# Kernel optimization log

Measured on AMD Instinct MI355X. Metric: run time of the kernel, lower is better.

## Reference

```python
import jax, jax.numpy as jnp
import numpy as np

HIDDEN = 1024
INNER = 1024
LR = 0.01
EPS = 1e-5


def _layernorm(x, gamma, beta):
    mu = jnp.mean(x, axis=-1, keepdims=True)
    var = jnp.var(x, axis=-1, keepdims=True)
    return (x - mu) * jax.lax.rsqrt(var + EPS) * gamma + beta


def setup_inputs() -> dict:
    key = jax.random.key(0)
    ks = jax.random.split(key, 8)
    B, S, H, I = 64, 512, HIDDEN, INNER
    x = jax.random.normal(ks[0], (B, S, H), dtype=jnp.float32)
    W_init = jax.random.normal(ks[1], (H, I), dtype=jnp.float32) * 0.02
    b_init = jnp.zeros((I,), dtype=jnp.float32)
    # Linear weights stored as (in, out) so y = x @ W + b
    lim_t = 1.0 / np.sqrt(H)
    Wt = jax.random.uniform(ks[2], (H, I), jnp.float32, -lim_t, lim_t)
    bt = jnp.zeros((I,), dtype=jnp.float32)
    lim_o = 1.0 / np.sqrt(I)
    Wo = jax.random.uniform(ks[3], (I, H), jnp.float32, -lim_o, lim_o)
    bo = jnp.zeros((H,), dtype=jnp.float32)
    lim_g = 1.0 / np.sqrt(2 * H)
    Wg = jax.random.uniform(ks[4], (2 * H, H), jnp.float32, -lim_g, lim_g)
    bg = jnp.zeros((H,), dtype=jnp.float32)
    gamma = jnp.ones((H,), dtype=jnp.float32)
    beta = jnp.zeros((H,), dtype=jnp.float32)
    return {"x": x, "W_init": W_init, "b_init": b_init, "Wt": Wt, "bt": bt,
            "Wo": Wo, "bo": bo, "Wg": Wg, "bg": bg, "gamma": gamma, "beta": beta}


def reference(x, W_init, b_init, Wt, bt, Wo, bo, Wg, bg, gamma, beta):
    B, S, H = x.shape
    I = W_init.shape[1]
    W0 = jnp.broadcast_to(W_init[None], (B, H, I))  # per-batch fast weights
    b0 = jnp.broadcast_to(b_init[None], (B, I))

    def step(carry, x_t):
        W, b = carry
        inner = jnp.einsum('bh,bhi->bi', x_t, W) + b          # [B, I]
        ttt = jax.nn.silu(inner) @ Wo + bo                    # [B, H]
        g = jax.nn.sigmoid(jnp.concatenate([x_t, ttt], axis=-1) @ Wg + bg)
        out = _layernorm(g * ttt + (1.0 - g) * x_t, gamma, beta)
        # test-time training update (target detached)
        target = jax.lax.stop_gradient(x_t @ Wt + bt)
        err = inner - target                                   # [B, I]
        W = W - (LR / I) * x_t[:, :, None] * err[:, None, :]
        b = b - (LR / I) * err
        return (W, b), out

    xs = jnp.swapaxes(x, 0, 1)  # [S, B, H]
    (_, _), ys = jax.lax.scan(step, (W0, b0), xs)
    return jnp.swapaxes(ys, 0, 1)  # [B, S, H]
```

## Files before the change

kernel.cpp:

```cpp
#include <hip/hip_runtime.h>

#define HD 1024
#define ID 1024
#define BATCH 64
#define SEQ 512
#define BS (BATCH*SEQ)
#define CHUNK 64
#define NCHUNK (SEQ/CHUNK)
#define LR_OVER_I (0.01f/1024.0f)

typedef unsigned int u32;
typedef unsigned short ushort_t;
typedef __attribute__((ext_vector_type(8))) short short8;
typedef __attribute__((ext_vector_type(8))) unsigned short ushort8;
typedef __attribute__((ext_vector_type(4))) unsigned short ushort4v;
typedef __attribute__((ext_vector_type(4))) float floatx4;

__device__ inline ushort_t f2bf(float f) {
    union { float f; u32 u; } v; v.f = f;
    return (ushort_t)((v.u + 0x7FFFu + ((v.u >> 16) & 1u)) >> 16);
}
__device__ inline float bf2f(ushort_t h) {
    union { u32 u; float f; } v; v.u = ((u32)h) << 16; return v.f;
}

__device__ inline void load_lds16(const void* g, void* l) {
    __builtin_amdgcn_global_load_lds(
        (const __attribute__((address_space(1))) u32*)g,
        (__attribute__((address_space(3))) u32*)l, 16, 0, 0);
}

__global__ void prep_all(const float* __restrict__ x, ushort_t* __restrict__ xb,
                         const float* __restrict__ Wi, const float* __restrict__ Wt,
                         ushort_t* __restrict__ WdT, ushort_t* __restrict__ WtT,
                         const float* __restrict__ bi, const float* __restrict__ bt,
                         float* __restrict__ bd,
                         const float* __restrict__ Wo, const float* __restrict__ Wg,
                         ushort_t* __restrict__ WoT, ushort_t* __restrict__ WgT)
{
    __shared__ float t1[32][33], t2[32][33];
    int bid = blockIdx.x;
    const int tid = threadIdx.x;
    if (bid < 16384) {
        long i = ((long)bid * 256 + tid) * 8;
        float4 a = *(const float4*)(x + i);
        float4 b = *(const float4*)(x + i + 4);
        ushort8 o;
        o[0] = f2bf(a.x); o[1] = f2bf(a.y); o[2] = f2bf(a.z); o[3] = f2bf(a.w);
        o[4] = f2bf(b.x); o[5] = f2bf(b.y); o[6] = f2bf(b.z); o[7] = f2bf(b.w);
        *(ushort8*)(xb + i) = o;
        return;
    }
    bid -= 16384;
    const int tx = tid & 31, ty = tid >> 5;
    if (bid < 1024) {
        if (bid == 0)
            for (int i = tid; i < ID; i += 256) bd[i] = bi[i] - bt[i];
        int r0 = (bid >> 5) * 32, c0 = (bid & 31) * 32;
        for (int i = ty; i < 32; i += 8) {
            t1[i][tx] = Wi[(long)(r0 + i) * ID + c0 + tx];
            t2[i][tx] = Wt[(long)(r0 + i) * ID + c0 + tx];
        }
        __syncthreads();
        for (int i = ty; i < 32; i += 8) {
            float wi = t1[tx][i], wt = t2[tx][i];
            WdT[(long)(c0 + i) * HD + r0 + tx] = f2bf(wi - wt);
            WtT[(long)(c0 + i) * HD + r0 + tx] = f2bf(wt);
        }
        return;
    }
    bid -= 1024;
    int z = bid >> 10, tile = bid & 1023;
    const float* in; ushort_t* outp; int ldo;
    if (z == 0)      { in = Wo;                 outp = WoT;      ldo = ID; }
    else if (z == 1) { in = Wg;                 outp = WgT;      ldo = 2 * HD; }
    else             { in = Wg + (long)HD * HD; outp = WgT + HD; ldo = 2 * HD; }
    int r0 = (tile >> 5) * 32, c0 = (tile & 31) * 32;
    for (int i = ty; i < 32; i += 8)
        t1[i][tx] = in[(long)(r0 + i) * HD + c0 + tx];
    __syncthreads();
    for (int i = ty; i < 32; i += 8)
        outp[(long)(c0 + i) * ldo + r0 + tx] = f2bf(t1[tx][i]);
}

__global__ __launch_bounds__(256, 3) void gemm_bf16(
    const ushort_t* __restrict__ A0, long sA0, int lda0,
    const ushort_t* __restrict__ A1, long sA1, int lda1,
    const ushort_t* __restrict__ Bt, long sBb, int ldb,
    void* __restrict__ Cv, long sCb, int ldc,
    int KSEG, const float* __restrict__ bias,
    float alpha, float add0, int flags,
    const ushort_t* __restrict__ Bt2, void* __restrict__ Cv2,
    const float* __restrict__ bias2, int flags2)
{
    long zb = blockIdx.z;
    int fl = flags;
    if (flags & 16) {
        zb = 0;
        if (blockIdx.z == 1) { Bt = Bt2; Cv = Cv2; bias = bias2; fl = flags2; }
    }
    int bx, by;
    {
        int L = blockIdx.y * gridDim.x + blockIdx.x;
        if ((gridDim.y & 7) == 0) {
            int xcd = L & 7, g = L >> 3;
            bx = g % gridDim.x;
            by = (g / gridDim.x) * 8 + xcd;
        } else { bx = blockIdx.x; by = blockIdx.y; }
    }
    const int M0 = by * 128, N0 = bx * 128;
    if ((fl & 2) && N0 > M0) return;

    __shared__ ushort_t As[128 * 32];
    __shared__ ushort_t Bs[128 * 32];
    const int tid = threadIdx.x;
    const int wave = tid >> 6, lane = tid & 63;
    const int lr = lane & 15, lq = lane >> 4;
    const int wm = (wave & 1) * 64, wn = (wave >> 1) * 64;

    ushort_t* la0 = &As[(wave * 16)      * 32];
    ushort_t* la1 = &As[(wave * 16 + 64) * 32];
    ushort_t* lb0 = &Bs[(wave * 16)      * 32];
    ushort_t* lb1 = &Bs[(wave * 16 + 64) * 32];

    const ushort_t* gb0 = Bt + zb * sBb
                        + (long)(N0 + wave * 16 + (lane >> 2)) * ldb + (lane & 3) * 8;
    const ushort_t* gb1 = gb0 + 64L * ldb;

    floatx4 acc[4][4] = {};

    for (int seg = 0; seg < 2; ++seg) {
        const ushort_t* Ag = (seg == 0) ? A0 : A1;
        if (!Ag) break;
        const int lda = (seg == 0) ? lda0 : lda1;
        Ag += zb * ((seg == 0) ? sA0 : sA1);
        const ushort_t* ga0 = Ag + (long)(M0 + wave * 16 + (lane >> 2)) * lda + (lane & 3) * 8;
        const ushort_t* ga1 = ga0 + 64L * lda;

        for (int k0 = 0; k0 < KSEG; k0 += 32) {
            load_lds16(ga0, la0);
            load_lds16(ga1, la1);
            load_lds16(gb0, lb0);
            load_lds16(gb1, lb1);
            ga0 += 32; ga1 += 32; gb0 += 32; gb1 += 32;
            __syncthreads();
            short8 af[4], bf4[4];
#pragma unroll
            for (int i = 0; i < 4; ++i)
                af[i] = *(const short8*)&As[(wm + i * 16 + lr) * 32 + lq * 8];
#pragma unroll
            for (int j = 0; j < 4; ++j)
                bf4[j] = *(const short8*)&Bs[(wn + j * 16 + lr) * 32 + lq * 8];
#pragma unroll
            for (int i = 0; i < 4; ++i)
#pragma unroll
                for (int j = 0; j < 4; ++j)
                    acc[i][j] = __builtin_amdgcn_mfma_f32_16x16x32_bf16(
                        af[i], bf4[j], acc[i][j], 0, 0, 0);
            __syncthreads();
        }
    }

    float bv[4] = {0.f, 0.f, 0.f, 0.f};
    if (bias) {
#pragma unroll
        for (int j = 0; j < 4; ++j) bv[j] = bias[N0 + wn + j * 16 + lr];
    }
    if (fl & 1) {
        ushort_t* C = (ushort_t*)Cv + zb * sCb;
#pragma unroll
        for (int i = 0; i < 4; ++i)
#pragma unroll
            for (int r = 0; r < 4; ++r) {
                int row = M0 + wm + i * 16 + lq * 4 + r;
                ushort_t* cp = C + (long)row * ldc + N0 + wn + lr;
#pragma unroll
                for (int j = 0; j < 4; ++j)
                    cp[j * 16] = f2bf(alpha * acc[i][j][r] + add0 + bv[j]);
            }
    } else {
        if ((fl & 8) && wm) return;
        float* C = (float*)Cv + zb * sCb;
#pragma unroll
        for (int i = 0; i < 4; ++i)
#pragma unroll
            for (int r = 0; r < 4; ++r) {
                int row = M0 + wm + i * 16 + lq * 4 + r;
                float* cp = C + (long)row * ldc + N0 + wn + lr;
#pragma unroll
                for (int j = 0; j < 4; ++j) {
                    float val = alpha * acc[i][j][r] + add0 + bv[j];
                    if (fl & 4) val += cp[j * 16];
                    cp[j * 16] = val;
                }
            }
    }
}

__global__ __launch_bounds__(256) void solve_chunk(const float* __restrict__ u,
                                                   const ushort_t* __restrict__ gram,
                                                   ushort_t* __restrict__ ebt,
                                                   ushort_t* __restrict__ tgtb, int c)
{
    const int b = blockIdx.z;
    const int j0 = blockIdx.x << 8;
    const int t0 = c << 6;
    const int tid = threadIdx.x;
    const int wave = tid >> 6, lane = tid & 63;
    const int lr = lane & 15, lq = lane >> 4;

    __shared__ float Us[64][260];
    __shared__ __align__(16) char smem2[2][20480];
    float* Gs = (float*)smem2;

    const ushort_t* Gb = gram + (long)b * SEQ * SEQ + (long)t0 * SEQ;
    const float* Ub = u + (long)b * SEQ * ID + (long)t0 * ID;
    ushort_t* Eb = ebt + (long)b * ID * SEQ;

    {
        const int r0w = wave * 16;
#pragma unroll
        for (int r = 0; r < 16; ++r)
            load_lds16(Ub + (long)(r0w + r) * ID + j0 + (lane << 2), &Us[r0w + r][0]);
    }

    if (c > 0) {
        const int K = c << 6;
        floatx4 acc[4][4] = {};
        const int arow = wave * 16 + (lane >> 2);
        const int acol = (lane & 3) * 8;

        auto stage = [&](int bsel, int k0) {
            ushort_t* As_ = (ushort_t*)smem2[bsel];
            ushort_t* Bs_ = (ushort_t*)(smem2[bsel] + 4096);
            const ushort_t* ga = Gb + (long)arow * SEQ + acol + k0;
            const ushort_t* gb = Eb + (long)(j0 + arow) * SEQ + acol + k0;
            load_lds16(ga,               &As_[(wave * 16) * 32]);
            load_lds16(gb,               &Bs_[(wave * 16)       * 32]);
            load_lds16(gb + 64L * SEQ,   &Bs_[(64  + wave * 16) * 32]);
            load_lds16(gb + 128L * SEQ,  &Bs_[(128 + wave * 16) * 32]);
            load_lds16(gb + 192L * SEQ,  &Bs_[(192 + wave * 16) * 32]);
        };

        stage(0, 0);
        __syncthreads();
        int buf = 0;
        for (int k0 = 0; k0 < K; k0 += 32) {
            if (k0 + 32 < K) stage(buf ^ 1, k0 + 32);
            const ushort_t* As_ = (const ushort_t*)smem2[buf];
            const ushort_t* Bs_ = (const ushort_t*)(smem2[buf] + 4096);
            short8 af[4], bf4[4];
#pragma unroll
            for (int i = 0; i < 4; ++i)
                af[i] = *(const short8*)&As_[(i * 16 + lr) * 32 + lq * 8];
#pragma unroll
            for (int j = 0; j < 4; ++j)
                bf4[j] = *(const short8*)&Bs_[(wave * 64 + j * 16 + lr) * 32 + lq * 8];
#pragma unroll
            for (int i = 0; i < 4; ++i)
#pragma unroll
                for (int j = 0; j < 4; ++j)
                    acc[i][j] = __builtin_amdgcn_mfma_f32_16x16x32_bf16(
                        af[i], bf4[j], acc[i][j], 0, 0, 0);
            __syncthreads();
            buf ^= 1;
        }
#pragma unroll
        for (int i = 0; i < 4; ++i)
#pragma unroll
            for (int r = 0; r < 4; ++r) {
                int row = i * 16 + lq * 4 + r;
#pragma unroll
                for (int j = 0; j < 4; ++j)
                    Us[row][wave * 64 + j * 16 + lr] -= acc[i][j][r];
            }
    }

    for (int v = tid; v < 512; v += 256) {
        int row = v >> 3, col8 = (v & 7) << 3;
        ushort8 g8 = *(const ushort8*)(Gb + (long)row * SEQ + t0 + col8);
#pragma unroll
        for (int k = 0; k < 8; ++k) Gs[row * 64 + col8 + k] = bf2f(g8[k]);
    }
    __syncthreads();

    float e[64];
    e[0] = Us[0][tid];
#pragma unroll
    for (int t = 1; t < 64; ++t) {
        float v = Us[t][tid];
        float p0 = 0.f, p1 = 0.f, p2 = 0.f, p3 = 0.f;
#pragma unroll
        for (int s = 0; s + 3 < t; s += 4) {
            p0 = fmaf(Gs[t * 64 + s + 0], e[s + 0], p0);
            p1 = fmaf(Gs[t * 64 + s + 1], e[s + 1], p1);
            p2 = fmaf(Gs[t * 64 + s + 2], e[s + 2], p2);
            p3 = fmaf(Gs[t * 64 + s + 3], e[s + 3], p3);
        }
#pragma unroll
        for (int s = t & ~3; s < t; ++s)
            p0 = fmaf(Gs[t * 64 + s], e[s], p0);
        e[t] = v - ((p0 + p1) + (p2 + p3));
    }

    if (c < NCHUNK - 1) {
        ushort_t* EB = Eb + (long)(j0 + tid) * SEQ + t0;
#pragma unroll
        for (int g = 0; g < 8; ++g) {
            ushort8 o;
#pragma unroll
            for (int k = 0; k < 8; ++k) o[k] = f2bf(e[g * 8 + k]);
            *(ushort8*)(EB + g * 8) = o;
        }
    }

    ushort_t* Tp = tgtb + ((long)b * SEQ + t0) * ID + j0 + tid;
#pragma unroll
    for (int t = 0; t < 64; ++t) {
        float v = e[t] + bf2f(Tp[(long)t * ID]);
        Tp[(long)t * ID] = f2bf(v / (1.0f + __expf(-v)));
    }
}

__global__ __launch_bounds__(256) void gate_ln(
    const ushort_t* __restrict__ zb, const ushort_t* __restrict__ tttb,
    const float* __restrict__ x, const float* __restrict__ gamma,
    const float* __restrict__ bet, float* __restrict__ out)
{
    long base = (long)blockIdx.x * HD + threadIdx.x * 4;
    ushort4v zv4 = *(const ushort4v*)(zb + base);
    ushort4v tv4 = *(const ushort4v*)(tttb + base);
    float4 xv = *(const float4*)(x + base);
    float xr[4] = {xv.x, xv.y, xv.z, xv.w};
    float y[4];
#pragma unroll
    for (int k = 0; k < 4; ++k) {
        float g = 1.0f / (1.0f + __expf(-bf2f(zv4[k])));
        float t = bf2f(tv4[k]);
        y[k] = g * t + (1.0f - g) * xr[k];
    }
    float sum = y[0] + y[1] + y[2] + y[3];
    float sq  = y[0]*y[0] + y[1]*y[1] + y[2]*y[2] + y[3]*y[3];
#pragma unroll
    for (int off = 32; off > 0; off >>= 1) {
        sum += __shfl_down(sum, off);
        sq  += __shfl_down(sq, off);
    }
    __shared__ float s1[4], s2[4];
    int wid = threadIdx.x >> 6;
    if ((threadIdx.x & 63) == 0) { s1[wid] = sum; s2[wid] = sq; }
    __syncthreads();
    float tot = s1[0] + s1[1] + s1[2] + s1[3];
    float tsq = s2[0] + s2[1] + s2[2] + s2[3];
    float mu = tot * (1.0f / HD);
    float var = tsq * (1.0f / HD) - mu * mu;
    float rs = rsqrtf(var + 1e-5f);
    int col = threadIdx.x * 4;
    float4 ov;
    ov.x = (y[0] - mu) * rs * gamma[col + 0] + bet[col + 0];
    ov.y = (y[1] - mu) * rs * gamma[col + 1] + bet[col + 1];
    ov.z = (y[2] - mu) * rs * gamma[col + 2] + bet[col + 2];
    ov.w = (y[3] - mu) * rs * gamma[col + 3] + bet[col + 3];
    *(float4*)(out + base) = ov;
}

extern "C" void kernel_launch(void* const* d_in, const int* in_sizes, int n_in,
                              void* d_out, int out_size, void* d_ws, size_t ws_size,
                              hipStream_t stream)
{
    const float* x    = (const float*)d_in[0];
    const float* Wi   = (const float*)d_in[1];
    const float* bi   = (const float*)d_in[2];
    const float* Wt   = (const float*)d_in[3];
    const float* bt   = (const float*)d_in[4];
    const float* Wo   = (const float*)d_in[5];
    const float* bo   = (const float*)d_in[6];
    const float* Wg   = (const float*)d_in[7];
    const float* bg   = (const float*)d_in[8];
    const float* gam  = (const float*)d_in[9];
    const float* bet  = (const float*)d_in[10];
    float* out = (float*)d_out;

    float* u       = (float*)d_ws;
    ushort_t* tgtb = (ushort_t*)(u + (long)BS * ID);
    float* gram    = (float*)(tgtb + (long)BS * ID);
    ushort_t* xb   = (ushort_t*)(gram + (long)BATCH * SEQ * SEQ);
    ushort_t* tttb = xb + (long)BS * HD;
    ushort_t* WdT  = tttb + (long)BS * HD;
    ushort_t* WtT  = WdT + (long)HD * ID;
    ushort_t* WoT  = WtT + (long)HD * ID;
    ushort_t* WgT  = WoT + (long)HD * ID;
    float* bd      = (float*)(WgT + (long)HD * 2 * HD);
    ushort_t* gramb = (ushort_t*)gram;
    ushort_t* ebt   = (ushort_t*)tttb;
    ushort_t* hb    = tgtb;
    ushort_t* zb    = (ushort_t*)u;

    prep_all<<<16384 + 1024 + 3072, 256, 0, stream>>>(
        x, xb, Wi, Wt, WdT, WtT, bi, bt, bd, Wo, Wg, WoT, WgT);

    dim3 gBig(ID / 128, BS / 128, 1);
    gemm_bf16<<<dim3(ID / 128, BS / 128, 2), 256, 0, stream>>>(
        xb, 0, HD, nullptr, 0, 0, WdT, 0, HD,
        u, 0, ID, HD, bd, 1.f, 0.f, 16,
        WtT, tgtb, bt, 1);
    gemm_bf16<<<dim3(SEQ / 128, SEQ / 128, BATCH), 256, 0, stream>>>(
        xb, (long)SEQ * HD, HD, nullptr, 0, 0, xb, (long)SEQ * HD, HD,
        gramb, (long)SEQ * SEQ, SEQ, HD, nullptr, LR_OVER_I, LR_OVER_I, 2 | 1,
        nullptr, nullptr, nullptr, 0);

    for (int c = 0; c < NCHUNK; ++c)
        solve_chunk<<<dim3(4, 1, BATCH), 256, 0, stream>>>(u, gramb, ebt, tgtb, c);

    gemm_bf16<<<gBig, 256, 0, stream>>>(hb, 0, ID, nullptr, 0, 0, WoT, 0, ID,
                                        tttb, 0, HD, ID, bo, 1.f, 0.f, 1,
                                        nullptr, nullptr, nullptr, 0);
    gemm_bf16<<<gBig, 256, 0, stream>>>(xb, 0, HD, tttb, 0, HD, WgT, 0, 2 * HD,
                                        zb, 0, HD, HD, bg, 1.f, 0.f, 1,
                                        nullptr, nullptr, nullptr, 0);
    gate_ln<<<BS, 256, 0, stream>>>(zb, tttb, x, gam, bet, out);
}
```

Baseline: 1.047 ms.

## Double solve_chunk block to 512 threads and split GEMM and epilogue work

Raises solve_chunk from 256 to 512 threads per block. The 8 waves now each compute a 64x32 slice of the correction GEMM instead of a 64x64 slice, and the Us and Gram staging loads are spread across more waves. The triangular solve still runs on only the first 256 threads, which write their results back to LDS. Then all 512 threads share the bf16 error store and the SiLU target epilogue, each handling half the timesteps. This is meant to add parallelism and latency hiding to a launch-bound kernel that has only 256 blocks, at the cost of an extra barrier, an LDS round trip, and half the threads idling during the serial solve.

```diff
diff --git a/kernel.cpp b/kernel.cpp
--- a/kernel.cpp
+++ b/kernel.cpp
@@ -197,7 +197,7 @@
     }
 }
 
-__global__ __launch_bounds__(256) void solve_chunk(const float* __restrict__ u,
+__global__ __launch_bounds__(512) void solve_chunk(const float* __restrict__ u,
                                                    const ushort_t* __restrict__ gram,
                                                    ushort_t* __restrict__ ebt,
                                                    ushort_t* __restrict__ tgtb, int c)
@@ -218,28 +218,28 @@
     ushort_t* Eb = ebt + (long)b * ID * SEQ;
 
     {
-        const int r0w = wave * 16;
-#pragma unroll
-        for (int r = 0; r < 16; ++r)
+        const int r0w = wave * 8;
+#pragma unroll
+        for (int r = 0; r < 8; ++r)
             load_lds16(Ub + (long)(r0w + r) * ID + j0 + (lane << 2), &Us[r0w + r][0]);
     }
 
     if (c > 0) {
         const int K = c << 6;
-        floatx4 acc[4][4] = {};
-        const int arow = wave * 16 + (lane >> 2);
-        const int acol = (lane & 3) * 8;
+        floatx4 acc[4][2] = {};
+        const int brow = wave * 32;
+        const int srow = lane >> 2, scol = (lane & 3) * 8;
 
         auto stage = [&](int bsel, int k0) {
             ushort_t* As_ = (ushort_t*)smem2[bsel];
             ushort_t* Bs_ = (ushort_t*)(smem2[bsel] + 4096);
-            const ushort_t* ga = Gb + (long)arow * SEQ + acol + k0;
-            const ushort_t* gb = Eb + (long)(j0 + arow) * SEQ + acol + k0;
-            load_lds16(ga,               &As_[(wave * 16) * 32]);
-            load_lds16(gb,               &Bs_[(wave * 16)       * 32]);
-            load_lds16(gb + 64L * SEQ,   &Bs_[(64  + wave * 16) * 32]);
-            load_lds16(gb + 128L * SEQ,  &Bs_[(128 + wave * 16) * 32]);
-            load_lds16(gb + 192L * SEQ,  &Bs_[(192 + wave * 16) * 32]);
+            if (wave < 4)
+                load_lds16(Gb + (long)(wave * 16 + srow) * SEQ + scol + k0,
+                           &As_[(wave * 16) * 32]);
+            load_lds16(Eb + (long)(j0 + brow + srow) * SEQ + scol + k0,
+                       &Bs_[(brow) * 32]);
+            load_lds16(Eb + (long)(j0 + brow + 16 + srow) * SEQ + scol + k0,
+                       &Bs_[(brow + 16) * 32]);
         };
 
         stage(0, 0);
@@ -249,19 +249,19 @@
             if (k0 + 32 < K) stage(buf ^ 1, k0 + 32);
             const ushort_t* As_ = (const ushort_t*)smem2[buf];
             const ushort_t* Bs_ = (const ushort_t*)(smem2[buf] + 4096);
-            short8 af[4], bf4[4];
+            short8 af[4], bfr[2];
 #pragma unroll
             for (int i = 0; i < 4; ++i)
                 af[i] = *(const short8*)&As_[(i * 16 + lr) * 32 + lq * 8];
 #pragma unroll
-            for (int j = 0; j < 4; ++j)
-                bf4[j] = *(const short8*)&Bs_[(wave * 64 + j * 16 + lr) * 32 + lq * 8];
+            for (int j = 0; j < 2; ++j)
+                bfr[j] = *(const short8*)&Bs_[(brow + j * 16 + lr) * 32 + lq * 8];
 #pragma unroll
             for (int i = 0; i < 4; ++i)
 #pragma unroll
-                for (int j = 0; j < 4; ++j)
+                for (int j = 0; j < 2; ++j)
                     acc[i][j] = __builtin_amdgcn_mfma_f32_16x16x32_bf16(
-                        af[i], bf4[j], acc[i][j], 0, 0, 0);
+                        af[i], bfr[j], acc[i][j], 0, 0, 0);
             __syncthreads();
             buf ^= 1;
         }
@@ -271,53 +271,60 @@
             for (int r = 0; r < 4; ++r) {
                 int row = i * 16 + lq * 4 + r;
 #pragma unroll
-                for (int j = 0; j < 4; ++j)
-                    Us[row][wave * 64 + j * 16 + lr] -= acc[i][j][r];
+                for (int j = 0; j < 2; ++j)
+                    Us[row][brow + j * 16 + lr] -= acc[i][j][r];
             }
     }
 
-    for (int v = tid; v < 512; v += 256) {
-        int row = v >> 3, col8 = (v & 7) << 3;
+    if (tid < 512) {
+        int row = tid >> 3, col8 = (tid & 7) << 3;
         ushort8 g8 = *(const ushort8*)(Gb + (long)row * SEQ + t0 + col8);
 #pragma unroll
         for (int k = 0; k < 8; ++k) Gs[row * 64 + col8 + k] = bf2f(g8[k]);
     }
     __syncthreads();
 
-    float e[64];
-    e[0] = Us[0][tid];
-#pragma unroll
-    for (int t = 1; t < 64; ++t) {
-        float v = Us[t][tid];
-        float p0 = 0.f, p1 = 0.f, p2 = 0.f, p3 = 0.f;
-#pragma unroll
-        for (int s = 0; s + 3 < t; s += 4) {
-            p0 = fmaf(Gs[t * 64 + s + 0], e[s + 0], p0);
-            p1 = fmaf(Gs[t * 64 + s + 1], e[s + 1], p1);
-            p2 = fmaf(Gs[t * 64 + s + 2], e[s + 2], p2);
-            p3 = fmaf(Gs[t * 64 + s + 3], e[s + 3], p3);
-        }
-#pragma unroll
-        for (int s = t & ~3; s < t; ++s)
-            p0 = fmaf(Gs[t * 64 + s], e[s], p0);
-        e[t] = v - ((p0 + p1) + (p2 + p3));
-    }
+    if (tid < 256) {
+        float e[64];
+        e[0] = Us[0][tid];
+#pragma unroll
+        for (int t = 1; t < 64; ++t) {
+            float v = Us[t][tid];
+            float p0 = 0.f, p1 = 0.f, p2 = 0.f, p3 = 0.f;
+#pragma unroll
+            for (int s = 0; s + 3 < t; s += 4) {
+                p0 = fmaf(Gs[t * 64 + s + 0], e[s + 0], p0);
+                p1 = fmaf(Gs[t * 64 + s + 1], e[s + 1], p1);
+                p2 = fmaf(Gs[t * 64 + s + 2], e[s + 2], p2);
+                p3 = fmaf(Gs[t * 64 + s + 3], e[s + 3], p3);
+            }
+#pragma unroll
+            for (int s = t & ~3; s < t; ++s)
+                p0 = fmaf(Gs[t * 64 + s], e[s], p0);
+            e[t] = v - ((p0 + p1) + (p2 + p3));
+        }
+#pragma unroll
+        for (int t = 0; t < 64; ++t) Us[t][tid] = e[t];
+    }
+    __syncthreads();
+
+    const int col = tid & 255, half = tid >> 8;
 
     if (c < NCHUNK - 1) {
-        ushort_t* EB = Eb + (long)(j0 + tid) * SEQ + t0;
-#pragma unroll
-        for (int g = 0; g < 8; ++g) {
+        ushort_t* EB = Eb + (long)(j0 + col) * SEQ + t0 + half * 32;
+#pragma unroll
+        for (int g = 0; g < 4; ++g) {
             ushort8 o;
 #pragma unroll
-            for (int k = 0; k < 8; ++k) o[k] = f2bf(e[g * 8 + k]);
+            for (int k = 0; k < 8; ++k) o[k] = f2bf(Us[half * 32 + g * 8 + k][col]);
             *(ushort8*)(EB + g * 8) = o;
         }
     }
 
-    ushort_t* Tp = tgtb + ((long)b * SEQ + t0) * ID + j0 + tid;
-#pragma unroll
-    for (int t = 0; t < 64; ++t) {
-        float v = e[t] + bf2f(Tp[(long)t * ID]);
+    ushort_t* Tp = tgtb + ((long)b * SEQ + t0 + half * 32) * ID + j0 + col;
+#pragma unroll
+    for (int t = 0; t < 32; ++t) {
+        float v = Us[half * 32 + t][col] + bf2f(Tp[(long)t * ID]);
         Tp[(long)t * ID] = f2bf(v / (1.0f + __expf(-v)));
     }
 }
@@ -410,7 +417,7 @@
         nullptr, nullptr, nullptr, 0);
 
     for (int c = 0; c < NCHUNK; ++c)
-        solve_chunk<<<dim3(4, 1, BATCH), 256, 0, stream>>>(u, gramb, ebt, tgtb, c);
+        solve_chunk<<<dim3(4, 1, BATCH), 512, 0, stream>>>(u, gramb, ebt, tgtb, c);
 
     gemm_bf16<<<gBig, 256, 0, stream>>>(hb, 0, ID, nullptr, 0, 0, WoT, 0, ID,
                                         tttb, 0, HD, ID, bo, 1.f, 0.f, 1,
```

Measured after the change: 1.035 ms. No clear change (-1.1%).
